# Kernel optimization log

Hardware: AMD Instinct MI355X
Metric: run time of the kernel (lower is better)

The kernel has to match this reference:

```python
import jax, jax.numpy as jnp
import numpy as np

N_NODES = 100000
N_EDGES = 3200000
NEG_SLOPE = 0.2  # PyG GATConv default
EPS = 1e-16      # PyG softmax denominator guard


def setup_inputs() -> dict:
    key = jax.random.key(0)
    ks = jax.random.split(key, 12)
    x = jax.random.normal(ks[0], (N_NODES, 4), dtype=jnp.float32)
    edge_index = jax.random.randint(ks[1], (2, N_EDGES), 0, N_NODES, dtype=jnp.int32)
    # conv1: in=4, heads=4, out=16, concat -> 64
    W1 = jax.random.normal(ks[2], (4, 64), dtype=jnp.float32) * 0.5
    a_src1 = jax.random.normal(ks[3], (4, 16), dtype=jnp.float32) * 0.3
    a_dst1 = jax.random.normal(ks[4], (4, 16), dtype=jnp.float32) * 0.3
    b1 = jnp.zeros((64,), dtype=jnp.float32)
    # conv2: in=64, heads=1, out=2, no concat
    W2 = jax.random.normal(ks[5], (64, 2), dtype=jnp.float32) * 0.2
    a_src2 = jax.random.normal(ks[6], (1, 2), dtype=jnp.float32) * 0.3
    a_dst2 = jax.random.normal(ks[7], (1, 2), dtype=jnp.float32) * 0.3
    b2 = jnp.zeros((2,), dtype=jnp.float32)
    return dict(x=x, edge_index=edge_index, W1=W1, a_src1=a_src1, a_dst1=a_dst1,
                b1=b1, W2=W2, a_src2=a_src2, a_dst2=a_dst2, b2=b2)


def _gat_layer(h_in, src, dst, W, a_s, a_d, b, heads, out_dim, concat):
    n = h_in.shape[0]
    h = (h_in @ W).reshape(n, heads, out_dim)            # [N, H, F]
    alpha_s = jnp.einsum('nhf,hf->nh', h, a_s)           # [N, H]
    alpha_d = jnp.einsum('nhf,hf->nh', h, a_d)
    e = jax.nn.leaky_relu(alpha_s[src] + alpha_d[dst], NEG_SLOPE)  # [E, H]
    # segment softmax over incoming edges of each dst node
    m = jax.ops.segment_max(e, dst, num_segments=n)      # [N, H]
    e = jnp.exp(e - m[dst])
    s = jax.ops.segment_sum(e, dst, num_segments=n)
    alpha = e / (s[dst] + EPS)                            # [E, H]
    msg = h[src] * alpha[:, :, None]                      # [E, H, F]
    out = jax.ops.segment_sum(msg, dst, num_segments=n)   # [N, H, F]
    if concat:
        out = out.reshape(n, heads * out_dim)
    else:
        out = out.mean(axis=1)
    return out + b


def reference(x, edge_index, W1, a_src1, a_dst1, b1, W2, a_src2, a_dst2, b2):
    n = x.shape[0]
    loop = jnp.arange(n, dtype=edge_index.dtype)
    src = jnp.concatenate([edge_index[0], loop])  # PyG add_self_loops=True
    dst = jnp.concatenate([edge_index[1], loop])
    h = jax.nn.elu(_gat_layer(x, src, dst, W1, a_src1, a_dst1, b1, 4, 16, True))
    h = _gat_layer(h, src, dst, W2, a_src2, a_dst2, b2, 1, 2, False)
    return jax.nn.log_softmax(h, axis=1)
```

## Files before the change

kernel.cpp:

```cpp
#include <hip/hip_runtime.h>
#include <hip/hip_fp16.h>
#include <math.h>

#define NEG_SLOPE 0.2f
#define EPS_F 1e-16f

#define P1_NB 256
#define P1_THREADS 256

__device__ __forceinline__ float leaky(float v) {
    return v >= 0.f ? v : NEG_SLOPE * v;
}


__global__ void k_p1hist(const int* __restrict__ dst, int* __restrict__ histT,
                         int E, int chunk, int nbucket) {
    __shared__ int cnt[256];
    int blk = blockIdx.x, t = threadIdx.x;
    cnt[t] = 0;
    __syncthreads();
    int s = blk * chunk, e = min(E, s + chunk);
    for (int i = s + t; i < e; i += P1_THREADS)
        atomicAdd(&cnt[dst[i] >> 9], 1);
    __syncthreads();
    if (t < nbucket) histT[t * P1_NB + blk] = cnt[t];
}

__global__ void k_scan1(const int* __restrict__ in, int* __restrict__ out,
                        int* __restrict__ blockSums, int M) {
    __shared__ int sdata[256];
    int t = threadIdx.x;
    int base = blockIdx.x * 1024 + t * 4;
    int v[4];
#pragma unroll
    for (int k = 0; k < 4; ++k) {
        int idx = base + k;
        v[k] = (idx < M) ? in[idx] : 0;
    }
    int total = v[0] + v[1] + v[2] + v[3];
    sdata[t] = total;
    __syncthreads();
    for (int off = 1; off < 256; off <<= 1) {
        int x = (t >= off) ? sdata[t - off] : 0;
        __syncthreads();
        sdata[t] += x;
        __syncthreads();
    }
    int run = sdata[t] - total;
#pragma unroll
    for (int k = 0; k < 4; ++k) {
        int idx = base + k;
        if (idx < M) out[idx] = run;
        run += v[k];
    }
    if (t == 255) blockSums[blockIdx.x] = sdata[255];
}

__global__ void k_scan2(int* __restrict__ blockSums, int nb) {
    __shared__ int sdata[256];
    int t = threadIdx.x;
    int val = (t < nb) ? blockSums[t] : 0;
    sdata[t] = val;
    __syncthreads();
    for (int off = 1; off < 256; off <<= 1) {
        int x = (t >= off) ? sdata[t - off] : 0;
        __syncthreads();
        sdata[t] += x;
        __syncthreads();
    }
    if (t < nb) blockSums[t] = sdata[t] - val;
}

__global__ void k_scan3g(int* __restrict__ out, const int* __restrict__ blockSums, int M) {
    int t = threadIdx.x;
    int base = blockIdx.x * 1024 + t * 4;
    int off = blockSums[blockIdx.x];
#pragma unroll
    for (int k = 0; k < 4; ++k) {
        int idx = base + k;
        if (idx < M) out[idx] += off;
    }
}

__global__ void k_p1scatter(const int* __restrict__ src, const int* __restrict__ dst,
                            const int* __restrict__ baseT, unsigned int* __restrict__ packed,
                            int E, int chunk, int nbucket) {
    __shared__ int cnt[256];
    int blk = blockIdx.x, t = threadIdx.x;
    if (t < nbucket) cnt[t] = baseT[t * P1_NB + blk];
    __syncthreads();
    int s = blk * chunk, e = min(E, s + chunk);
    for (int i = s + t; i < e; i += P1_THREADS) {
        int d = dst[i];
        int pos = atomicAdd(&cnt[d >> 9], 1);
        packed[pos] = ((unsigned int)(d & 511) << 23) | (unsigned int)src[i];
    }
}

__global__ void k_fine(const unsigned int* __restrict__ packed, const int* __restrict__ baseT,
                       int* __restrict__ csr, int* __restrict__ rowptr, int N, int E) {
    __shared__ int cnt[512];
    __shared__ int sc[512];
    int b = blockIdx.x, t = threadIdx.x;
    int nbucket = gridDim.x;
    int startE = baseT[b * P1_NB];
    int endE = (b == nbucket - 1) ? E : baseT[(b + 1) * P1_NB];

    if (t < 512) cnt[t] = 0;
    __syncthreads();
    for (int i = startE + t; i < endE; i += 1024)
        atomicAdd(&cnt[packed[i] >> 23], 1);
    __syncthreads();
    if (t < 512) sc[t] = cnt[t];
    __syncthreads();
    for (int off = 1; off < 512; off <<= 1) {
        int v = (t < 512 && t >= off) ? sc[t - off] : 0;
        __syncthreads();
        if (t < 512) sc[t] += v;
        __syncthreads();
    }
    if (t < 512) {
        int excl = sc[t] - cnt[t];
        int node = (b << 9) + t;
        if (node < N) rowptr[node] = startE + excl;
        cnt[t] = excl;
    }
    if (b == 0 && t == 0) rowptr[N] = E;
    __syncthreads();
    for (int i = startE + t; i < endE; i += 1024) {
        unsigned int p = packed[i];
        int pos = startE + atomicAdd(&cnt[p >> 23], 1);
        csr[pos] = (int)(p & 0x7FFFFFu);
    }
}

__global__ void k_phaseA(const float* __restrict__ x, const float* __restrict__ W1,
                         const float* __restrict__ a_src1, const float* __restrict__ a_dst1,
                         __half* __restrict__ h1h, float* __restrict__ as1,
                         float* __restrict__ ad1, int N) {
    int node = blockIdx.x * 4 + (threadIdx.x >> 6);
    if (node >= N) return;
    int lane = threadIdx.x & 63;
    float x0 = x[node * 4 + 0], x1 = x[node * 4 + 1];
    float x2 = x[node * 4 + 2], x3 = x[node * 4 + 3];
    float h = x0 * W1[lane] + x1 * W1[64 + lane] + x2 * W1[128 + lane] + x3 * W1[192 + lane];
    h1h[(size_t)node * 64 + lane] = __float2half(h);
    float as = h * a_src1[lane];
    float ad = h * a_dst1[lane];
#pragma unroll
    for (int m = 8; m >= 1; m >>= 1) {
        as += __shfl_xor(as, m, 16);
        ad += __shfl_xor(ad, m, 16);
    }
    if ((lane & 15) == 0) {
        int head = lane >> 4;
        as1[node * 4 + head] = as;
        ad1[node * 4 + head] = ad;
    }
}

__global__ void k_layer1(const int* __restrict__ rowptr, const int* __restrict__ csr,
                         const __half* __restrict__ h1h, const float* __restrict__ as1,
                         const float* __restrict__ ad1, const float* __restrict__ b1,
                         const float* __restrict__ W2, const float* __restrict__ a_src2,
                         const float* __restrict__ a_dst2,
                         float4* __restrict__ node2, int N) {
    int node = blockIdx.x * 4 + (threadIdx.x >> 6);
    if (node >= N) return;
    int lane = threadIdx.x & 63;
    int head4 = lane & 3;
    int j     = lane >> 2;
    int sub   = lane >> 4;
    int fl    = lane & 15;
    int h     = fl >> 2;

    int beg = rowptr[node], end = rowptr[node + 1];

    float ad_s1 = ad1[node * 4 + head4];
    float pself4 = __expf(leaky(as1[node * 4 + head4] + ad_s1));
    float psum = (lane < 4) ? pself4 : 0.f;

    float pselfF = __shfl(pself4, h);
    float a0 = 0.f, a1 = 0.f, a2 = 0.f, a3 = 0.f;
    if (sub == 0) {
        float2 raw = *(const float2*)(h1h + ((size_t)node << 6) + (fl << 2));
        __half2 h01 = *reinterpret_cast<__half2*>(&raw.x);
        __half2 h23 = *reinterpret_cast<__half2*>(&raw.y);
        float2 f01 = __half22float2(h01), f23 = __half22float2(h23);
        a0 = pselfF * f01.x; a1 = pselfF * f01.y;
        a2 = pselfF * f23.x; a3 = pselfF * f23.y;
    }

    for (int c = beg; c < end; c += 16) {
        int e = c + j;
        bool valid = e < end;
        int s = csr[valid ? e : beg];
        float v = leaky(as1[s * 4 + head4] + ad_s1);
        float p = valid ? __expf(v) : 0.f;
        psum += p;

        int s_q[4];
#pragma unroll
        for (int m = 0; m < 4; ++m) s_q[m] = __shfl(s, m * 16 + sub * 4);
        float2 raw[4];
#pragma unroll
        for (int m = 0; m < 4; ++m)
            raw[m] = *(const float2*)(h1h + ((size_t)s_q[m] << 6) + (fl << 2));
        float p_q[4];
#pragma unroll
        for (int m = 0; m < 4; ++m) p_q[m] = __shfl(p, m * 16 + sub * 4 + h);
#pragma unroll
        for (int m = 0; m < 4; ++m) {
            __half2 h01 = *reinterpret_cast<__half2*>(&raw[m].x);
            __half2 h23 = *reinterpret_cast<__half2*>(&raw[m].y);
            float2 f01 = __half22float2(h01), f23 = __half22float2(h23);
            a0 = fmaf(p_q[m], f01.x, a0);
            a1 = fmaf(p_q[m], f01.y, a1);
            a2 = fmaf(p_q[m], f23.x, a2);
            a3 = fmaf(p_q[m], f23.y, a3);
        }
    }

    a0 += __shfl_xor(a0, 16); a0 += __shfl_xor(a0, 32);
    a1 += __shfl_xor(a1, 16); a1 += __shfl_xor(a1, 32);
    a2 += __shfl_xor(a2, 16); a2 += __shfl_xor(a2, 32);
    a3 += __shfl_xor(a3, 16); a3 += __shfl_xor(a3, 32);

#pragma unroll
    for (int m = 4; m <= 32; m <<= 1) psum += __shfl_xor(psum, m);
    float psumF = __shfl(psum, h);
    float inv = 1.f / (psumF + EPS_F);

    float4 b1v = ((const float4*)b1)[fl];
    float o0 = a0 * inv + b1v.x;
    float o1 = a1 * inv + b1v.y;
    float o2 = a2 * inv + b1v.z;
    float o3 = a3 * inv + b1v.w;
    float e0 = o0 > 0.f ? o0 : expm1f(o0);
    float e1 = o1 > 0.f ? o1 : expm1f(o1);
    float e2 = o2 > 0.f ? o2 : expm1f(o2);
    float e3 = o3 > 0.f ? o3 : expm1f(o3);

    float4 w01 = ((const float4*)W2)[fl * 2];
    float4 w23 = ((const float4*)W2)[fl * 2 + 1];
    float c0 = e0 * w01.x + e1 * w01.z + e2 * w23.x + e3 * w23.z;
    float c1 = e0 * w01.y + e1 * w01.w + e2 * w23.y + e3 * w23.w;
#pragma unroll
    for (int m = 8; m >= 1; m >>= 1) {
        c0 += __shfl_xor(c0, m);
        c1 += __shfl_xor(c1, m);
    }
    if (lane == 0) {
        float as2 = c0 * a_src2[0] + c1 * a_src2[1];
        float ad2 = c0 * a_dst2[0] + c1 * a_dst2[1];
        node2[node] = make_float4(c0, c1, as2, ad2);
    }
}

__global__ void k_layer2(const int* __restrict__ rowptr, const int* __restrict__ csr,
                         const float4* __restrict__ node2, const float* __restrict__ b2,
                         float* __restrict__ out, int N) {
    int node = blockIdx.x * 4 + (threadIdx.x >> 6);
    if (node >= N) return;
    int lane = threadIdx.x & 63;

    float4 me = node2[node];
    float ad = me.w;
    int beg = rowptr[node], end = rowptr[node + 1];

    float psum = 0.f, a0 = 0.f, a1 = 0.f;
    for (int e = beg + lane; e < end; e += 64) {
        float4 sn = node2[csr[e]];
        float p = __expf(leaky(sn.z + ad));
        psum += p;
        a0 = fmaf(p, sn.x, a0);
        a1 = fmaf(p, sn.y, a1);
    }
    if (lane == 0) {
        float p = __expf(leaky(me.z + ad));
        psum += p;
        a0 = fmaf(p, me.x, a0);
        a1 = fmaf(p, me.y, a1);
    }
#pragma unroll
    for (int m = 32; m >= 1; m >>= 1) {
        psum += __shfl_xor(psum, m);
        a0 += __shfl_xor(a0, m);
        a1 += __shfl_xor(a1, m);
    }
    if (lane == 0) {
        float inv = 1.f / (psum + EPS_F);
        float o0 = a0 * inv + b2[0];
        float o1 = a1 * inv + b2[1];
        float mx = fmaxf(o0, o1);
        float lse = mx + logf(__expf(o0 - mx) + __expf(o1 - mx));
        out[node * 2 + 0] = o0 - lse;
        out[node * 2 + 1] = o1 - lse;
    }
}


extern "C" void kernel_launch(void* const* d_in, const int* in_sizes, int n_in,
                              void* d_out, int out_size, void* d_ws, size_t ws_size,
                              hipStream_t stream) {
    const float* x      = (const float*)d_in[0];
    const int*   ei     = (const int*)d_in[1];
    const float* W1     = (const float*)d_in[2];
    const float* a_src1 = (const float*)d_in[3];
    const float* a_dst1 = (const float*)d_in[4];
    const float* b1     = (const float*)d_in[5];
    const float* W2     = (const float*)d_in[6];
    const float* a_src2 = (const float*)d_in[7];
    const float* a_dst2 = (const float*)d_in[8];
    const float* b2     = (const float*)d_in[9];
    float* out = (float*)d_out;

    int N = in_sizes[0] / 4;
    int E = in_sizes[1] / 2;
    const int* e_src = ei;
    const int* e_dst = ei + E;

    int nbucket = (N + 511) >> 9;
    int M = nbucket * P1_NB;

    char* w = (char*)d_ws;
    auto alloc = [&](size_t bytes) -> void* {
        void* p = (void*)w;
        w += (bytes + 255) & ~(size_t)255;
        return p;
    };
    __half* h1h       = (__half*)alloc((size_t)N * 64 * 2);
    float*  as1       = (float*)alloc((size_t)N * 4 * 4);
    float*  ad1       = (float*)alloc((size_t)N * 4 * 4);
    float4* node2     = (float4*)alloc((size_t)N * 16);
    int*    rowptr    = (int*)alloc((size_t)(N + 1) * 4);
    int*    histT     = (int*)alloc((size_t)M * 4);
    int*    baseT     = (int*)alloc((size_t)M * 4);
    int*    blockSums = (int*)alloc(256 * 4);
    int*    csr       = (int*)alloc((size_t)E * 4);
    unsigned int* packed = (unsigned int*)alloc((size_t)E * 4);

    int chunk = (E + P1_NB - 1) / P1_NB;
    int nbScan = (M + 1023) / 1024;
    int nodeb = (N + 3) / 4;

    k_p1hist<<<P1_NB, P1_THREADS, 0, stream>>>(e_dst, histT, E, chunk, nbucket);
    k_scan1<<<nbScan, 256, 0, stream>>>(histT, baseT, blockSums, M);
    k_scan2<<<1, 256, 0, stream>>>(blockSums, nbScan);
    k_scan3g<<<nbScan, 256, 0, stream>>>(baseT, blockSums, M);
    k_p1scatter<<<P1_NB, P1_THREADS, 0, stream>>>(e_src, e_dst, baseT, packed, E, chunk, nbucket);
    k_fine<<<nbucket, 1024, 0, stream>>>(packed, baseT, csr, rowptr, N, E);

    k_phaseA<<<nodeb, 256, 0, stream>>>(x, W1, a_src1, a_dst1, h1h, as1, ad1, N);
    k_layer1<<<nodeb, 256, 0, stream>>>(rowptr, csr, h1h, as1, ad1, b1, W2,
                                        a_src2, a_dst2, node2, N);
    k_layer2<<<nodeb, 256, 0, stream>>>(rowptr, csr, node2, b2, out, N);
}
```

Before: 282.3 us.

## Precompute per-edge attention weights in CSR build and simplify layer1 gather

Moves the layer-1 attention logit and exp computation into the fine CSR-building kernel, which now runs after phaseA so it can read the per-node source and destination scores. Each edge gets four half-precision unnormalized weights (shifted by a constant to avoid overflow) stored alongside its CSR entry. Layer1 then reads these weights directly instead of gathering as1 and doing exp per edge, and it drops the shuffle-based broadcasting of source indices and weights. The cost is an extra 8 bytes per edge written and read. The fp16 weights with a fixed shift lose precision and can underflow or overflow for extreme logits.

Result: slower. 338.5 us (+19.9%).

```diff
diff --git a/kernel.cpp b/kernel.cpp
--- a/kernel.cpp
+++ b/kernel.cpp
@@ -4,6 +4,7 @@
 
 #define NEG_SLOPE 0.2f
 #define EPS_F 1e-16f
+#define PSHIFT 9.0f
 
 #define P1_NB 256
 #define P1_THREADS 256
@@ -98,15 +99,22 @@
 }
 
 __global__ void k_fine(const unsigned int* __restrict__ packed, const int* __restrict__ baseT,
-                       int* __restrict__ csr, int* __restrict__ rowptr, int N, int E) {
+                       const float* __restrict__ as1, const float* __restrict__ ad1,
+                       int* __restrict__ csr, uint2* __restrict__ prec,
+                       int* __restrict__ rowptr, int N, int E) {
     __shared__ int cnt[512];
     __shared__ int sc[512];
+    __shared__ float4 adc[512];
     int b = blockIdx.x, t = threadIdx.x;
     int nbucket = gridDim.x;
     int startE = baseT[b * P1_NB];
     int endE = (b == nbucket - 1) ? E : baseT[(b + 1) * P1_NB];
 
-    if (t < 512) cnt[t] = 0;
+    if (t < 512) {
+        cnt[t] = 0;
+        int node = (b << 9) + t;
+        adc[t] = (node < N) ? ((const float4*)ad1)[node] : make_float4(0.f, 0.f, 0.f, 0.f);
+    }
     __syncthreads();
     for (int i = startE + t; i < endE; i += 1024)
         atomicAdd(&cnt[packed[i] >> 23], 1);
@@ -129,8 +137,19 @@
     __syncthreads();
     for (int i = startE + t; i < endE; i += 1024) {
         unsigned int p = packed[i];
-        int pos = startE + atomicAdd(&cnt[p >> 23], 1);
-        csr[pos] = (int)(p & 0x7FFFFFu);
+        int local = (int)(p >> 23);
+        int srcv = (int)(p & 0x7FFFFFu);
+        int pos = startE + atomicAdd(&cnt[local], 1);
+        float4 as4 = ((const float4*)as1)[srcv];
+        float4 ad4 = adc[local];
+        float p0 = __expf(leaky(as4.x + ad4.x) - PSHIFT);
+        float p1 = __expf(leaky(as4.y + ad4.y) - PSHIFT);
+        float p2 = __expf(leaky(as4.z + ad4.z) - PSHIFT);
+        float p3 = __expf(leaky(as4.w + ad4.w) - PSHIFT);
+        __half2 h01 = __floats2half2_rn(p0, p1);
+        __half2 h23 = __floats2half2_rn(p2, p3);
+        csr[pos] = srcv;
+        prec[pos] = make_uint2(*(unsigned int*)&h01, *(unsigned int*)&h23);
     }
 }
 
@@ -160,64 +179,44 @@
 }
 
 __global__ void k_layer1(const int* __restrict__ rowptr, const int* __restrict__ csr,
-                         const __half* __restrict__ h1h, const float* __restrict__ as1,
-                         const float* __restrict__ ad1, const float* __restrict__ b1,
-                         const float* __restrict__ W2, const float* __restrict__ a_src2,
-                         const float* __restrict__ a_dst2,
+                         const uint2* __restrict__ prec, const __half* __restrict__ h1h,
+                         const float* __restrict__ as1, const float* __restrict__ ad1,
+                         const float* __restrict__ b1, const float* __restrict__ W2,
+                         const float* __restrict__ a_src2, const float* __restrict__ a_dst2,
                          float4* __restrict__ node2, int N) {
     int node = blockIdx.x * 4 + (threadIdx.x >> 6);
     if (node >= N) return;
     int lane = threadIdx.x & 63;
-    int head4 = lane & 3;
-    int j     = lane >> 2;
-    int sub   = lane >> 4;
-    int fl    = lane & 15;
-    int h     = fl >> 2;
+    int sub = lane >> 4;
+    int fl  = lane & 15;
+    int h   = fl >> 2;
 
     int beg = rowptr[node], end = rowptr[node + 1];
 
-    float ad_s1 = ad1[node * 4 + head4];
-    float pself4 = __expf(leaky(as1[node * 4 + head4] + ad_s1));
-    float psum = (lane < 4) ? pself4 : 0.f;
-
-    float pselfF = __shfl(pself4, h);
     float a0 = 0.f, a1 = 0.f, a2 = 0.f, a3 = 0.f;
-    if (sub == 0) {
-        float2 raw = *(const float2*)(h1h + ((size_t)node << 6) + (fl << 2));
-        __half2 h01 = *reinterpret_cast<__half2*>(&raw.x);
-        __half2 h23 = *reinterpret_cast<__half2*>(&raw.y);
-        float2 f01 = __half22float2(h01), f23 = __half22float2(h23);
-        a0 = pselfF * f01.x; a1 = pselfF * f01.y;
-        a2 = pselfF * f23.x; a3 = pselfF * f23.y;
-    }
+    float psum = 0.f;
 
     for (int c = beg; c < end; c += 16) {
-        int e = c + j;
-        bool valid = e < end;
-        int s = csr[valid ? e : beg];
-        float v = leaky(as1[s * 4 + head4] + ad_s1);
-        float p = valid ? __expf(v) : 0.f;
-        psum += p;
-
-        int s_q[4];
-#pragma unroll
-        for (int m = 0; m < 4; ++m) s_q[m] = __shfl(s, m * 16 + sub * 4);
-        float2 raw[4];
-#pragma unroll
-        for (int m = 0; m < 4; ++m)
-            raw[m] = *(const float2*)(h1h + ((size_t)s_q[m] << 6) + (fl << 2));
-        float p_q[4];
-#pragma unroll
-        for (int m = 0; m < 4; ++m) p_q[m] = __shfl(p, m * 16 + sub * 4 + h);
+        int ebase = c + sub * 4;
 #pragma unroll
         for (int m = 0; m < 4; ++m) {
-            __half2 h01 = *reinterpret_cast<__half2*>(&raw[m].x);
-            __half2 h23 = *reinterpret_cast<__half2*>(&raw[m].y);
-            float2 f01 = __half22float2(h01), f23 = __half22float2(h23);
-            a0 = fmaf(p_q[m], f01.x, a0);
-            a1 = fmaf(p_q[m], f01.y, a1);
-            a2 = fmaf(p_q[m], f23.x, a2);
-            a3 = fmaf(p_q[m], f23.y, a3);
+            int e = ebase + m;
+            bool valid = e < end;
+            int ec = valid ? e : beg;
+            int s = csr[ec];
+            uint2 pr = prec[ec];
+            unsigned int pair = (h < 2) ? pr.x : pr.y;
+            unsigned short pu = (h & 1) ? (unsigned short)(pair >> 16)
+                                        : (unsigned short)(pair & 0xFFFFu);
+            float p = valid ? __half2float(__ushort_as_half(pu)) : 0.f;
+            psum += p;
+            float2 raw = *(const float2*)(h1h + ((size_t)s << 6) + (fl << 2));
+            __half2 h01 = *reinterpret_cast<__half2*>(&raw.x);
+            __half2 h23 = *reinterpret_cast<__half2*>(&raw.y);
+            a0 = fmaf(p, __half2float(__low2half(h01)), a0);
+            a1 = fmaf(p, __half2float(__high2half(h01)), a1);
+            a2 = fmaf(p, __half2float(__low2half(h23)), a2);
+            a3 = fmaf(p, __half2float(__high2half(h23)), a3);
         }
     }
 
@@ -225,12 +224,21 @@
     a1 += __shfl_xor(a1, 16); a1 += __shfl_xor(a1, 32);
     a2 += __shfl_xor(a2, 16); a2 += __shfl_xor(a2, 32);
     a3 += __shfl_xor(a3, 16); a3 += __shfl_xor(a3, 32);
-
-#pragma unroll
-    for (int m = 4; m <= 32; m <<= 1) psum += __shfl_xor(psum, m);
-    float psumF = __shfl(psum, h);
-    float inv = 1.f / (psumF + EPS_F);
-
+    psum += __shfl_xor(psum, 16); psum += __shfl_xor(psum, 32);
+
+    float pself = __expf(leaky(as1[node * 4 + h] + ad1[node * 4 + h]) - PSHIFT);
+    psum += pself;
+    {
+        float2 raw = *(const float2*)(h1h + ((size_t)node << 6) + (fl << 2));
+        __half2 h01 = *reinterpret_cast<__half2*>(&raw.x);
+        __half2 h23 = *reinterpret_cast<__half2*>(&raw.y);
+        a0 = fmaf(pself, __half2float(__low2half(h01)), a0);
+        a1 = fmaf(pself, __half2float(__high2half(h01)), a1);
+        a2 = fmaf(pself, __half2float(__low2half(h23)), a2);
+        a3 = fmaf(pself, __half2float(__high2half(h23)), a3);
+    }
+
+    float inv = 1.f / (psum + EPS_F);
     float4 b1v = ((const float4*)b1)[fl];
     float o0 = a0 * inv + b1v.x;
     float o1 = a1 * inv + b1v.y;
@@ -339,20 +347,21 @@
     int*    blockSums = (int*)alloc(256 * 4);
     int*    csr       = (int*)alloc((size_t)E * 4);
     unsigned int* packed = (unsigned int*)alloc((size_t)E * 4);
+    uint2*  prec      = (uint2*)alloc((size_t)E * 8);
 
     int chunk = (E + P1_NB - 1) / P1_NB;
     int nbScan = (M + 1023) / 1024;
     int nodeb = (N + 3) / 4;
 
+    k_phaseA<<<nodeb, 256, 0, stream>>>(x, W1, a_src1, a_dst1, h1h, as1, ad1, N);
     k_p1hist<<<P1_NB, P1_THREADS, 0, stream>>>(e_dst, histT, E, chunk, nbucket);
     k_scan1<<<nbScan, 256, 0, stream>>>(histT, baseT, blockSums, M);
     k_scan2<<<1, 256, 0, stream>>>(blockSums, nbScan);
     k_scan3g<<<nbScan, 256, 0, stream>>>(baseT, blockSums, M);
     k_p1scatter<<<P1_NB, P1_THREADS, 0, stream>>>(e_src, e_dst, baseT, packed, E, chunk, nbucket);
-    k_fine<<<nbucket, 1024, 0, stream>>>(packed, baseT, csr, rowptr, N, E);
-
-    k_phaseA<<<nodeb, 256, 0, stream>>>(x, W1, a_src1, a_dst1, h1h, as1, ad1, N);
-    k_layer1<<<nodeb, 256, 0, stream>>>(rowptr, csr, h1h, as1, ad1, b1, W2,
+    k_fine<<<nbucket, 1024, 0, stream>>>(packed, baseT, as1, ad1, csr, prec, rowptr, N, E);
+
+    k_layer1<<<nodeb, 256, 0, stream>>>(rowptr, csr, prec, h1h, as1, ad1, b1, W2,
                                         a_src2, a_dst2, node2, N);
     k_layer2<<<nodeb, 256, 0, stream>>>(rowptr, csr, node2, b2, out, N);
 }
```
